# Kernel optimization log

Hardware: AMD Instinct MI355X
Metric: run time of the kernel (lower is better)

## Reference

```python
import jax, jax.numpy as jnp
import numpy as np

D = 65536
N_T, N_G, N_L = 256, 256, 1024


def setup_inputs() -> dict:
    key = jax.random.key(0)
    k1, k2, k3 = jax.random.split(key, 3)
    return {
        "out_student_global": jax.random.normal(k1, (N_G, D), dtype=jnp.float32),
        "out_student_local": jax.random.normal(k2, (N_L, D), dtype=jnp.float32),
        "out_teacher": jax.random.normal(k3, (N_T, D), dtype=jnp.float32),
        "center": jnp.zeros((1, D), dtype=jnp.float32),
        "temp_student": jnp.array([0.1], dtype=jnp.float32),
        "temp_teacher": jnp.array([0.04], dtype=jnp.float32),
        "cent_rate_m": jnp.array([0.9], dtype=jnp.float32),
    }


def reference(out_student_global, out_student_local, out_teacher, center,
              temp_student, temp_teacher, cent_rate_m):
    # Student log-probabilities (log_softmax of each part, then concat --
    # identical to concat-then-log_softmax since softmax is row-wise).
    log_prob_s_g = jax.nn.log_softmax(out_student_global / temp_student, axis=-1)
    log_prob_s_l = jax.nn.log_softmax(out_student_local / temp_student, axis=-1)
    log_prob_s = jnp.concatenate([log_prob_s_g, log_prob_s_l], axis=0)  # [Ns, D]
    # Teacher probabilities with centering.
    prob_t = jax.nn.softmax((out_teacher - center) / temp_teacher, axis=-1)  # [Nt, D]
    # All pairwise cross-entropies in one matmul: ce[i, j] = -sum_d p_t[i,d] * log q_s[j,d]
    ce = -jnp.einsum('td,sd->ts', prob_t, log_prob_s)  # [Nt, Ns]
    n_t, n_s = ce.shape
    diag_mask = jnp.arange(n_t)[:, None] == jnp.arange(n_s)[None, :]  # skip i == j
    total_loss = jnp.sum(jnp.where(diag_mask, jnp.zeros((), ce.dtype), ce))
    n_loss_terms = n_t * n_s - min(n_t, n_s)  # static count of off-diagonal pairs
    return total_loss / n_loss_terms
```

## Files before the change

### kernel.cpp

```cpp
#include <hip/hip_runtime.h>
#include <math.h>

#define D 65536
#define NT 256
#define NG 256
#define NL 1024
#define NS 1280
#define CT 32
#define TILE_W 2048
#define RG 40
#define KC_SPLIT 8

typedef float vfloat4 __attribute__((ext_vector_type(4)));


__device__ __forceinline__ float max4(vfloat4 v) {
    return fmaxf(fmaxf(v.x, v.y), fmaxf(v.z, v.w));
}

__global__ __launch_bounds__(256) void kA(const float* __restrict__ sg,
                                          const float* __restrict__ sl,
                                          const float* __restrict__ tempS,
                                          float* __restrict__ Sxs,
                                          float* __restrict__ partial,
                                          float2* __restrict__ stats,
                                          int use_atomic) {
    const int tid  = threadIdx.x;
    const int lane = tid & 63;
    const int w    = tid >> 6;
    const int ct   = blockIdx.x;
    const int gy   = blockIdx.y;
    const int c0   = ct * TILE_W;
    const float invTs = 1.0f / tempS[0];
    const bool is_local = (gy >= 8);

    __shared__ float lds_sx[4][TILE_W];

    vfloat4 sx[8];
    #pragma unroll
    for (int j = 0; j < 8; ++j) sx[j] = (vfloat4)0.0f;

    for (int i = 0; i < 4; ++i) {
        const int rA = gy * 32 + i * 8 + w;
        const int rB = rA + 4;
        const float* rowA = is_local ? (sl + (size_t)(rA - NG) * D) : (sg + (size_t)rA * D);
        const float* rowB = is_local ? (sl + (size_t)(rB - NG) * D) : (sg + (size_t)rB * D);
        const vfloat4* pA = (const vfloat4*)(rowA + c0) + lane;
        const vfloat4* pB = (const vfloat4*)(rowB + c0) + lane;

        float mA = -INFINITY, zA = 0.0f;
        float mB = -INFINITY, zB = 0.0f;
        #pragma unroll
        for (int h = 0; h < 2; ++h) {
            vfloat4 a[4], b[4];
            #pragma unroll
            for (int j = 0; j < 4; ++j) {
                const vfloat4* qa = pA + (h * 4 + j) * 64;
                const vfloat4* qb = pB + (h * 4 + j) * 64;
                a[j] = is_local ? __builtin_nontemporal_load(qa) : *qa;
                b[j] = is_local ? __builtin_nontemporal_load(qb) : *qb;
            }
            #pragma unroll
            for (int j = 0; j < 4; ++j) {
                const vfloat4 ua = a[j] * invTs;
                const vfloat4 ub = b[j] * invTs;
                sx[h * 4 + j] += ua + ub;
                const float mnA = fmaxf(mA, max4(ua));
                const float mnB = fmaxf(mB, max4(ub));
                const float fa = (__expf(ua.x - mnA) + __expf(ua.y - mnA))
                               + (__expf(ua.z - mnA) + __expf(ua.w - mnA));
                const float fb = (__expf(ub.x - mnB) + __expf(ub.y - mnB))
                               + (__expf(ub.z - mnB) + __expf(ub.w - mnB));
                zA = zA * __expf(mA - mnA) + fa;
                zB = zB * __expf(mB - mnB) + fb;
                mA = mnA;
                mB = mnB;
            }
        }
        #pragma unroll
        for (int off = 32; off; off >>= 1) {
            const float mA2 = __shfl_xor(mA, off, 64);
            const float zA2 = __shfl_xor(zA, off, 64);
            const float mB2 = __shfl_xor(mB, off, 64);
            const float zB2 = __shfl_xor(zB, off, 64);
            const float mnA = fmaxf(mA, mA2);
            const float mnB = fmaxf(mB, mB2);
            zA = zA * __expf(mA - mnA) + zA2 * __expf(mA2 - mnA);
            zB = zB * __expf(mB - mnB) + zB2 * __expf(mB2 - mnB);
            mA = mnA;
            mB = mnB;
        }
        if (lane == 0) {
            stats[(size_t)rA * CT + ct] = make_float2(mA, zA);
            stats[(size_t)rB * CT + ct] = make_float2(mB, zB);
        }
    }

    #pragma unroll
    for (int ch = 0; ch < 8; ++ch)
        ((vfloat4*)&lds_sx[w][ch * 256])[lane] = sx[ch];
    __syncthreads();

    #pragma unroll
    for (int k = 0; k < 2; ++k) {
        const int i4 = k * 256 + tid;
        vfloat4 v = ((vfloat4*)lds_sx[0])[i4] + ((vfloat4*)lds_sx[1])[i4]
                  + ((vfloat4*)lds_sx[2])[i4] + ((vfloat4*)lds_sx[3])[i4];
        if (use_atomic) {
            const int c = c0 + i4 * 4;
            atomicAdd(&Sxs[c + 0], v.x);
            atomicAdd(&Sxs[c + 1], v.y);
            atomicAdd(&Sxs[c + 2], v.z);
            atomicAdd(&Sxs[c + 3], v.w);
        } else {
            ((vfloat4*)(partial + (size_t)gy * D + c0))[i4] = v;
        }
    }
}

__global__ __launch_bounds__(256) void kB(const float* __restrict__ partial,
                                          float* __restrict__ Sxs) {
    const int col = blockIdx.x * 256 + threadIdx.x;
    float s = 0.0f;
    #pragma unroll 8
    for (int g = 0; g < RG; ++g) s += partial[(size_t)g * D + col];
    Sxs[col] = s;
}

__global__ __launch_bounds__(256) void kC(const float* __restrict__ tch,
                                          const float* __restrict__ sg,
                                          const float* __restrict__ center,
                                          const float* __restrict__ Sxs,
                                          const float* __restrict__ tempS,
                                          const float* __restrict__ tempT,
                                          float4* __restrict__ tup) {
    const int t   = blockIdx.x >> 3;
    const int q   = blockIdx.x & 7;
    const int tid = threadIdx.x;
    const float invTt = 1.0f / tempT[0];
    const float invTs = 1.0f / tempS[0];

    const vfloat4* xt = (const vfloat4*)(tch + (size_t)t * D);
    const vfloat4* xg = (const vfloat4*)(sg  + (size_t)t * D);
    const float4*  c4 = (const float4*)center;
    const float4*  s4 = (const float4*)Sxs;

    float m = -INFINITY, Z = 0.0f, A = 0.0f, Dg = 0.0f;
    const int base = q * (D / 4 / KC_SPLIT);
    #pragma unroll 2
    for (int it = 0; it < (D / 4 / KC_SPLIT) / 256; ++it) {
        const int idx = base + it * 256 + tid;
        const vfloat4 x = __builtin_nontemporal_load(xt + idx);
        const vfloat4 g = __builtin_nontemporal_load(xg + idx);
        const float4  c = c4[idx];
        const float4  s = s4[idx];
        const float y0 = (x.x - c.x) * invTt, y1 = (x.y - c.y) * invTt;
        const float y2 = (x.z - c.z) * invTt, y3 = (x.w - c.w) * invTt;
        const float mn = fmaxf(m, fmaxf(fmaxf(y0, y1), fmaxf(y2, y3)));
        const float sc = __expf(m - mn);
        const float f0 = __expf(y0 - mn), f1 = __expf(y1 - mn);
        const float f2 = __expf(y2 - mn), f3 = __expf(y3 - mn);
        Z  = Z  * sc + ((f0 + f1) + (f2 + f3));
        A  = A  * sc + ((f0 * s.x + f1 * s.y) + (f2 * s.z + f3 * s.w));
        Dg = Dg * sc + ((f0 * g.x + f1 * g.y) + (f2 * g.z + f3 * g.w)) * invTs;
        m  = mn;
    }
    #pragma unroll
    for (int off = 32; off; off >>= 1) {
        const float m2 = __shfl_xor(m,  off, 64);
        const float Z2 = __shfl_xor(Z,  off, 64);
        const float A2 = __shfl_xor(A,  off, 64);
        const float G2 = __shfl_xor(Dg, off, 64);
        const float mn = fmaxf(m, m2);
        const float s1 = __expf(m  - mn);
        const float s2 = __expf(m2 - mn);
        Z  = Z  * s1 + Z2 * s2;
        A  = A  * s1 + A2 * s2;
        Dg = Dg * s1 + G2 * s2;
        m  = mn;
    }
    __shared__ float4 lds[4];
    const int w = tid >> 6, lane = tid & 63;
    if (lane == 0) lds[w] = make_float4(m, Z, A, Dg);
    __syncthreads();
    if (tid == 0) {
        float4 r = lds[0];
        for (int k = 1; k < 4; ++k) {
            const float4 p = lds[k];
            const float mn = fmaxf(r.x, p.x);
            const float s1 = __expf(r.x - mn);
            const float s2 = __expf(p.x - mn);
            r = make_float4(mn, r.y*s1 + p.y*s2, r.z*s1 + p.z*s2, r.w*s1 + p.w*s2);
        }
        tup[blockIdx.x] = r;
    }
}

__device__ __forceinline__ float2 merge2(float2 a, float2 b) {
    const float mn = fmaxf(a.x, b.x);
    return make_float2(mn, a.y * __expf(a.x - mn) + b.y * __expf(b.x - mn));
}

__global__ __launch_bounds__(256) void kD(const float2* __restrict__ stats,
                                          const float4* __restrict__ tup,
                                          float* __restrict__ out) {
    const int tid = threadIdx.x;
    float accC = 0.0f, accCg = 0.0f;
    for (int r = tid; r < NS; r += 256) {
        const float4* sp = (const float4*)(stats + (size_t)r * CT);
        float4 v[16];
        #pragma unroll
        for (int k = 0; k < 16; ++k) v[k] = sp[k];
        float2 p[16];
        #pragma unroll
        for (int k = 0; k < 16; ++k)
            p[k] = merge2(make_float2(v[k].x, v[k].y), make_float2(v[k].z, v[k].w));
        #pragma unroll
        for (int step = 8; step; step >>= 1)
            #pragma unroll
            for (int k = 0; k < step; ++k) p[k] = merge2(p[k], p[k + step]);
        const float l = p[0].x + logf(p[0].y);
        accC += l;
        if (r < NG) accCg += l;
    }
    float termS = 0.0f;
    if (tid < NT) {
        float4 r = tup[KC_SPLIT * tid];
        for (int k = 1; k < KC_SPLIT; ++k) {
            const float4 pp = tup[KC_SPLIT * tid + k];
            const float mn = fmaxf(r.x, pp.x);
            const float s1 = __expf(r.x - mn);
            const float s2 = __expf(pp.x - mn);
            r = make_float4(mn, r.y*s1 + pp.y*s2, r.z*s1 + pp.z*s2, r.w*s1 + pp.w*s2);
        }
        termS = (r.z - r.w) / r.y;
    }
    #pragma unroll
    for (int off = 32; off; off >>= 1) {
        accC  += __shfl_xor(accC,  off, 64);
        accCg += __shfl_xor(accCg, off, 64);
        termS += __shfl_xor(termS, off, 64);
    }
    __shared__ float l1[4], l2[4], l3[4];
    const int w = tid >> 6, lane = tid & 63;
    if (lane == 0) { l1[w] = accC; l2[w] = accCg; l3[w] = termS; }
    __syncthreads();
    if (tid == 0) {
        float C = 0.0f, Cg = 0.0f, S = 0.0f;
        for (int k = 0; k < 4; ++k) { C += l1[k]; Cg += l2[k]; S += l3[k]; }
        out[0] = (256.0f * C - Cg - S) * (1.0f / 327424.0f);
    }
}

extern "C" void kernel_launch(void* const* d_in, const int* in_sizes, int n_in,
                              void* d_out, int out_size, void* d_ws, size_t ws_size,
                              hipStream_t stream) {
    const float* sg     = (const float*)d_in[0];
    const float* sl     = (const float*)d_in[1];
    const float* tch    = (const float*)d_in[2];
    const float* center = (const float*)d_in[3];
    const float* tempS  = (const float*)d_in[4];
    const float* tempT  = (const float*)d_in[5];

    float* ws = (float*)d_ws;
    float*  Sxs     = ws;
    float2* stats   = (float2*)(ws + D);
    float4* tup     = (float4*)(ws + D + NS * CT * 2);
    float*  partial = ws + D + NS * CT * 2 + NT * KC_SPLIT * 4;

    const size_t needed = (size_t)(D + NS * CT * 2 + NT * KC_SPLIT * 4 + RG * D) * sizeof(float);
    const int use_atomic = (ws_size < needed) ? 1 : 0;

    if (use_atomic)
        hipMemsetAsync(Sxs, 0, D * sizeof(float), stream);
    kA<<<dim3(CT, RG), 256, 0, stream>>>(sg, sl, tempS, Sxs, partial, stats, use_atomic);
    if (!use_atomic)
        kB<<<D / 256, 256, 0, stream>>>(partial, Sxs);
    kC<<<NT * KC_SPLIT, 256, 0, stream>>>(tch, sg, center, Sxs, tempS, tempT, tup);
    kD<<<1, 256, 0, stream>>>(stats, tup, (float*)d_out);
}
```

Before: 480.6 us.

## Restructure kernel inner loops: one row per wave pass, vectorized reductions, dual accumulators

In kA each wave now handles one row per iteration across 8 iterations. It computes a single per-row max over the 8 loaded vectors and then one batch of exps, instead of an online rescale after every vector, which removes the repeated rescale exps. The nontemporal loads in kA and kC are replaced with plain loads. kB now sums float4 vectors with a quarter of the blocks, and kC keeps two independent online-softmax accumulators to expose more ILP. The cost is higher register pressure, and the plain loads may pollute the cache.

```diff
diff --git a/kernel.cpp b/kernel.cpp
--- a/kernel.cpp
+++ b/kernel.cpp
@@ -16,6 +16,18 @@
 
 __device__ __forceinline__ float max4(vfloat4 v) {
     return fmaxf(fmaxf(v.x, v.y), fmaxf(v.z, v.w));
+}
+__device__ __forceinline__ vfloat4 vmax4(vfloat4 a, vfloat4 b) {
+    vfloat4 r;
+    r.x = fmaxf(a.x, b.x); r.y = fmaxf(a.y, b.y);
+    r.z = fmaxf(a.z, b.z); r.w = fmaxf(a.w, b.w);
+    return r;
+}
+__device__ __forceinline__ vfloat4 exp4(vfloat4 v) {
+    vfloat4 r;
+    r.x = __expf(v.x); r.y = __expf(v.y);
+    r.z = __expf(v.z); r.w = __expf(v.w);
+    return r;
 }
 
 __global__ __launch_bounds__(256) void kA(const float* __restrict__ sg,
@@ -32,7 +44,8 @@
     const int gy   = blockIdx.y;
     const int c0   = ct * TILE_W;
     const float invTs = 1.0f / tempS[0];
-    const bool is_local = (gy >= 8);
+    const float* __restrict__ base =
+        (gy >= 8) ? (sl + (size_t)(gy - 8) * 32 * D) : (sg + (size_t)gy * 32 * D);
 
     __shared__ float lds_sx[4][TILE_W];
 
@@ -40,60 +53,34 @@
     #pragma unroll
     for (int j = 0; j < 8; ++j) sx[j] = (vfloat4)0.0f;
 
-    for (int i = 0; i < 4; ++i) {
-        const int rA = gy * 32 + i * 8 + w;
-        const int rB = rA + 4;
-        const float* rowA = is_local ? (sl + (size_t)(rA - NG) * D) : (sg + (size_t)rA * D);
-        const float* rowB = is_local ? (sl + (size_t)(rB - NG) * D) : (sg + (size_t)rB * D);
-        const vfloat4* pA = (const vfloat4*)(rowA + c0) + lane;
-        const vfloat4* pB = (const vfloat4*)(rowB + c0) + lane;
-
-        float mA = -INFINITY, zA = 0.0f;
-        float mB = -INFINITY, zB = 0.0f;
-        #pragma unroll
-        for (int h = 0; h < 2; ++h) {
-            vfloat4 a[4], b[4];
-            #pragma unroll
-            for (int j = 0; j < 4; ++j) {
-                const vfloat4* qa = pA + (h * 4 + j) * 64;
-                const vfloat4* qb = pB + (h * 4 + j) * 64;
-                a[j] = is_local ? __builtin_nontemporal_load(qa) : *qa;
-                b[j] = is_local ? __builtin_nontemporal_load(qb) : *qb;
-            }
-            #pragma unroll
-            for (int j = 0; j < 4; ++j) {
-                const vfloat4 ua = a[j] * invTs;
-                const vfloat4 ub = b[j] * invTs;
-                sx[h * 4 + j] += ua + ub;
-                const float mnA = fmaxf(mA, max4(ua));
-                const float mnB = fmaxf(mB, max4(ub));
-                const float fa = (__expf(ua.x - mnA) + __expf(ua.y - mnA))
-                               + (__expf(ua.z - mnA) + __expf(ua.w - mnA));
-                const float fb = (__expf(ub.x - mnB) + __expf(ub.y - mnB))
-                               + (__expf(ub.z - mnB) + __expf(ub.w - mnB));
-                zA = zA * __expf(mA - mnA) + fa;
-                zB = zB * __expf(mB - mnB) + fb;
-                mA = mnA;
-                mB = mnB;
-            }
-        }
+    #pragma unroll 2
+    for (int i = 0; i < 8; ++i) {
+        const int r = i * 4 + w;
+        const vfloat4* __restrict__ p = (const vfloat4*)(base + (size_t)r * D + c0) + lane;
+        vfloat4 x[8];
+        #pragma unroll
+        for (int j = 0; j < 8; ++j) x[j] = p[j * 64];
+        #pragma unroll
+        for (int j = 0; j < 8; ++j) { x[j] *= invTs; sx[j] += x[j]; }
+        const vfloat4 mx = vmax4(vmax4(vmax4(x[0], x[1]), vmax4(x[2], x[3])),
+                                 vmax4(vmax4(x[4], x[5]), vmax4(x[6], x[7])));
+        float m = max4(mx);
+        const vfloat4 e0 = exp4(x[0] - m), e1 = exp4(x[1] - m);
+        const vfloat4 e2 = exp4(x[2] - m), e3 = exp4(x[3] - m);
+        const vfloat4 e4 = exp4(x[4] - m), e5 = exp4(x[5] - m);
+        const vfloat4 e6 = exp4(x[6] - m), e7 = exp4(x[7] - m);
+        const vfloat4 es = ((e0 + e1) + (e2 + e3)) + ((e4 + e5) + (e6 + e7));
+        float z = (es.x + es.y) + (es.z + es.w);
         #pragma unroll
         for (int off = 32; off; off >>= 1) {
-            const float mA2 = __shfl_xor(mA, off, 64);
-            const float zA2 = __shfl_xor(zA, off, 64);
-            const float mB2 = __shfl_xor(mB, off, 64);
-            const float zB2 = __shfl_xor(zB, off, 64);
-            const float mnA = fmaxf(mA, mA2);
-            const float mnB = fmaxf(mB, mB2);
-            zA = zA * __expf(mA - mnA) + zA2 * __expf(mA2 - mnA);
-            zB = zB * __expf(mB - mnB) + zB2 * __expf(mB2 - mnB);
-            mA = mnA;
-            mB = mnB;
-        }
-        if (lane == 0) {
-            stats[(size_t)rA * CT + ct] = make_float2(mA, zA);
-            stats[(size_t)rB * CT + ct] = make_float2(mB, zB);
-        }
+            const float m2 = __shfl_xor(m, off, 64);
+            const float z2 = __shfl_xor(z, off, 64);
+            const float mn = fmaxf(m, m2);
+            z = z * __expf(m - mn) + z2 * __expf(m2 - mn);
+            m = mn;
+        }
+        if (lane == 0)
+            stats[(size_t)(gy * 32 + r) * CT + ct] = make_float2(m, z);
     }
 
     #pragma unroll
@@ -120,11 +107,12 @@
 
 __global__ __launch_bounds__(256) void kB(const float* __restrict__ partial,
                                           float* __restrict__ Sxs) {
-    const int col = blockIdx.x * 256 + threadIdx.x;
-    float s = 0.0f;
+    const int i4 = blockIdx.x * 256 + threadIdx.x;
+    const vfloat4* __restrict__ p = (const vfloat4*)partial;
+    vfloat4 s = (vfloat4)0.0f;
     #pragma unroll 8
-    for (int g = 0; g < RG; ++g) s += partial[(size_t)g * D + col];
-    Sxs[col] = s;
+    for (int g = 0; g < RG; ++g) s += p[(size_t)g * (D / 4) + i4];
+    ((vfloat4*)Sxs)[i4] = s;
 }
 
 __global__ __launch_bounds__(256) void kC(const float* __restrict__ tch,
@@ -140,31 +128,49 @@
     const float invTt = 1.0f / tempT[0];
     const float invTs = 1.0f / tempS[0];
 
-    const vfloat4* xt = (const vfloat4*)(tch + (size_t)t * D);
-    const vfloat4* xg = (const vfloat4*)(sg  + (size_t)t * D);
-    const float4*  c4 = (const float4*)center;
-    const float4*  s4 = (const float4*)Sxs;
-
-    float m = -INFINITY, Z = 0.0f, A = 0.0f, Dg = 0.0f;
+    const vfloat4* __restrict__ xt = (const vfloat4*)(tch + (size_t)t * D);
+    const vfloat4* __restrict__ xg = (const vfloat4*)(sg  + (size_t)t * D);
+    const vfloat4* __restrict__ c4 = (const vfloat4*)center;
+    const vfloat4* __restrict__ s4 = (const vfloat4*)Sxs;
+
     const int base = q * (D / 4 / KC_SPLIT);
-    #pragma unroll 2
-    for (int it = 0; it < (D / 4 / KC_SPLIT) / 256; ++it) {
-        const int idx = base + it * 256 + tid;
-        const vfloat4 x = __builtin_nontemporal_load(xt + idx);
-        const vfloat4 g = __builtin_nontemporal_load(xg + idx);
-        const float4  c = c4[idx];
-        const float4  s = s4[idx];
-        const float y0 = (x.x - c.x) * invTt, y1 = (x.y - c.y) * invTt;
-        const float y2 = (x.z - c.z) * invTt, y3 = (x.w - c.w) * invTt;
-        const float mn = fmaxf(m, fmaxf(fmaxf(y0, y1), fmaxf(y2, y3)));
-        const float sc = __expf(m - mn);
-        const float f0 = __expf(y0 - mn), f1 = __expf(y1 - mn);
-        const float f2 = __expf(y2 - mn), f3 = __expf(y3 - mn);
-        Z  = Z  * sc + ((f0 + f1) + (f2 + f3));
-        A  = A  * sc + ((f0 * s.x + f1 * s.y) + (f2 * s.z + f3 * s.w));
-        Dg = Dg * sc + ((f0 * g.x + f1 * g.y) + (f2 * g.z + f3 * g.w)) * invTs;
-        m  = mn;
-    }
+    float m0 = -INFINITY, Z0 = 0.0f, A0 = 0.0f, G0 = 0.0f;
+    float m1 = -INFINITY, Z1 = 0.0f, A1 = 0.0f, G1 = 0.0f;
+
+    #pragma unroll
+    for (int it = 0; it < (D / 4 / KC_SPLIT) / 256; it += 2) {
+        const int ia = base + it * 256 + tid;
+        const int ib = ia + 256;
+        const vfloat4 xa = xt[ia], ga = xg[ia], ca = c4[ia], sa = s4[ia];
+        const vfloat4 xb = xt[ib], gb = xg[ib], cb = c4[ib], sb = s4[ib];
+
+        const vfloat4 ya = (xa - ca) * invTt;
+        const float mna = fmaxf(m0, max4(ya));
+        const float sca = __expf(m0 - mna);
+        const vfloat4 fa = exp4(ya - mna);
+        Z0 = Z0 * sca + ((fa.x + fa.y) + (fa.z + fa.w));
+        A0 = A0 * sca + ((fa.x * sa.x + fa.y * sa.y) + (fa.z * sa.z + fa.w * sa.w));
+        G0 = G0 * sca + ((fa.x * ga.x + fa.y * ga.y) + (fa.z * ga.z + fa.w * ga.w));
+        m0 = mna;
+
+        const vfloat4 yb = (xb - cb) * invTt;
+        const float mnb = fmaxf(m1, max4(yb));
+        const float scb = __expf(m1 - mnb);
+        const vfloat4 fb = exp4(yb - mnb);
+        Z1 = Z1 * scb + ((fb.x + fb.y) + (fb.z + fb.w));
+        A1 = A1 * scb + ((fb.x * sb.x + fb.y * sb.y) + (fb.z * sb.z + fb.w * sb.w));
+        G1 = G1 * scb + ((fb.x * gb.x + fb.y * gb.y) + (fb.z * gb.z + fb.w * gb.w));
+        m1 = mnb;
+    }
+    float m = fmaxf(m0, m1);
+    {
+        const float s1 = __expf(m0 - m);
+        const float s2 = __expf(m1 - m);
+        Z0 = Z0 * s1 + Z1 * s2;
+        A0 = A0 * s1 + A1 * s2;
+        G0 = (G0 * s1 + G1 * s2) * invTs;
+    }
+    float Z = Z0, A = A0, Dg = G0;
     #pragma unroll
     for (int off = 32; off; off >>= 1) {
         const float m2 = __shfl_xor(m,  off, 64);
@@ -275,7 +281,7 @@
         hipMemsetAsync(Sxs, 0, D * sizeof(float), stream);
     kA<<<dim3(CT, RG), 256, 0, stream>>>(sg, sl, tempS, Sxs, partial, stats, use_atomic);
     if (!use_atomic)
-        kB<<<D / 256, 256, 0, stream>>>(partial, Sxs);
+        kB<<<D / 1024, 256, 0, stream>>>(partial, Sxs);
     kC<<<NT * KC_SPLIT, 256, 0, stream>>>(tch, sg, center, Sxs, tempS, tempT, tup);
     kD<<<1, 256, 0, stream>>>(stats, tup, (float*)d_out);
 }
```

Result: no change. 481.5 us (+0.2%).
